# Optimization experiments

Hardware: AMD Instinct MI355X
Metric: run time of the kernel (lower is better)

Reference implementation:

```python
import jax, jax.numpy as jnp
import numpy as np
from jax import lax

C = 256
HEADS = 8
AREA = 4
MLP_DIM = int(1.2 * C)  # 307


def _conv1x1(x, w, s, b):
    # x: [B,C,H,W], w: [O,C], s,b: [O]  (Conv2d 1x1 bias=False + folded BN)
    y = jnp.einsum('bchw,oc->bohw', x, w)
    return y * s[None, :, None, None] + b[None, :, None, None]


def _dwconv3x3(x, w, s, b):
    # depthwise 3x3, groups=C; w: [C,1,3,3]
    y = lax.conv_general_dilated(x, w, (1, 1), ((1, 1), (1, 1)),
                                 feature_group_count=x.shape[1],
                                 dimension_numbers=('NCHW', 'OIHW', 'NCHW'))
    return y * s[None, :, None, None] + b[None, :, None, None]


def setup_inputs() -> dict:
    key = jax.random.key(0)
    ks = jax.random.split(key, 8)
    B, H, W = 2, 64, 64
    x = jax.random.normal(ks[0], (B, C, H, W), dtype=jnp.float32)
    std = 0.02
    w_qk = jax.random.normal(ks[1], (2 * C, C), dtype=jnp.float32) * std
    w_v = jax.random.normal(ks[2], (C, C), dtype=jnp.float32) * std
    w_pe = jax.random.normal(ks[3], (C, 1, 3, 3), dtype=jnp.float32) * std
    w_proj = jax.random.normal(ks[4], (C, C), dtype=jnp.float32) * std
    w_m1 = jax.random.normal(ks[5], (MLP_DIM, C), dtype=jnp.float32) * std
    w_m2 = jax.random.normal(ks[6], (C, MLP_DIM), dtype=jnp.float32) * std
    ones = lambda n: jnp.ones((n,), jnp.float32)
    zeros = lambda n: jnp.zeros((n,), jnp.float32)
    return {
        'x': x,
        'w_qk': w_qk, 's_qk': ones(2 * C), 'b_qk': zeros(2 * C),
        'w_v': w_v, 's_v': ones(C), 'b_v': zeros(C),
        'w_pe': w_pe, 's_pe': ones(C), 'b_pe': zeros(C),
        'w_proj': w_proj, 's_proj': ones(C), 'b_proj': zeros(C),
        'w_m1': w_m1, 's_m1': ones(MLP_DIM), 'b_m1': zeros(MLP_DIM),
        'w_m2': w_m2, 's_m2': ones(C), 'b_m2': zeros(C),
    }


def _block(x, w_qk, s_qk, b_qk, w_v, s_v, b_v, w_pe, s_pe, b_pe,
           w_proj, s_proj, b_proj, w_m1, s_m1, b_m1, w_m2, s_m2, b_m2):
    B, Cc, H, W = x.shape
    N = H * W
    hd = Cc // HEADS
    scale = hd ** -0.5

    # --- AreaAttention ---
    qk = _conv1x1(x, w_qk, s_qk, b_qk).reshape(B, 2 * Cc, N)
    v4 = _conv1x1(x, w_v, s_v, b_v)                 # [B,C,H,W]
    pe = _dwconv3x3(v4, w_pe, s_pe, b_pe)           # positional encoding
    v = v4.reshape(B, Cc, N)

    # area split (row-major reshape, identical to torch contiguous reshape)
    Ba, Na = B * AREA, N // AREA
    qk = qk.reshape(Ba, 2 * Cc, Na)
    v = v.reshape(Ba, Cc, Na)
    q, k = qk[:, :Cc], qk[:, Cc:]
    q = q.reshape(Ba, HEADS, hd, Na)
    k = k.reshape(Ba, HEADS, hd, Na)
    v = v.reshape(Ba, HEADS, hd, Na)

    attn = jnp.einsum('bhdn,bhdm->bhnm', q, k) * scale  # [Ba,H,Na,Na]
    attn = jax.nn.softmax(attn, axis=-1)
    out = jnp.einsum('bhdm,bhnm->bhdn', v, attn)         # [Ba,H,hd,Na]

    out = out.reshape(B, Cc, N).reshape(B, Cc, H, W)
    attn_out = _conv1x1(out + pe, w_proj, s_proj, b_proj)

    x1 = x + attn_out  # add=True (shortcut and in_c==out_c)

    # --- conv2 MLP: Conv(SiLU) -> Conv(act=False) ---
    m = jax.nn.silu(_conv1x1(x1, w_m1, s_m1, b_m1))
    m = _conv1x1(m, w_m2, s_m2, b_m2)
    return x1 + m


def reference(x, w_qk, s_qk, b_qk, w_v, s_v, b_v, w_pe, s_pe, b_pe,
              w_proj, s_proj, b_proj, w_m1, s_m1, b_m1, w_m2, s_m2, b_m2):
    return _block(x, w_qk, s_qk, b_qk, w_v, s_v, b_v, w_pe, s_pe, b_pe,
                  w_proj, s_proj, b_proj, w_m1, s_m1, b_m1, w_m2, s_m2, b_m2)
```

## Files before the change

### kernel.cpp

```cpp
#include <hip/hip_runtime.h>

typedef __attribute__((ext_vector_type(8))) short s8v;
typedef __attribute__((ext_vector_type(4))) float f4v;

#define QSC (0.17677669529663687f * 1.4426950408889634f)

__device__ __forceinline__ unsigned short f2bf(float x) {
    unsigned u = __float_as_uint(x);
    return (unsigned short)((u + 0x7fffu + ((u >> 16) & 1u)) >> 16);
}
__device__ __forceinline__ float bf2f(unsigned short h) {
    return __uint_as_float(((unsigned)h) << 16);
}
__device__ __forceinline__ unsigned trunc2(float a, float b) {
    return (__float_as_uint(b) & 0xffff0000u) | (__float_as_uint(a) >> 16);
}

__global__ __launch_bounds__(256) void wconv_kernel(
    const float* __restrict__ wqk, const float* __restrict__ sqk, const float* __restrict__ bqk,
    const float* __restrict__ wv,  const float* __restrict__ sv,  const float* __restrict__ bv,
    const float* __restrict__ wprj, const float* __restrict__ sprj,
    const float* __restrict__ wm1, const float* __restrict__ sm1, const float* __restrict__ bm1,
    const float* __restrict__ wm2, const float* __restrict__ sm2,
    const float* __restrict__ wpe9,
    unsigned short* __restrict__ Wqkv, unsigned short* __restrict__ Wp,
    unsigned short* __restrict__ Wm1,  unsigned short* __restrict__ Wm2,
    float* __restrict__ bpad, float* __restrict__ bqv, float* __restrict__ wpeT)
{
    int i = blockIdx.x * 256 + threadIdx.x;
    if (i < 196608) {
        int o = i >> 8, c = i & 255;
        float w;
        if (o < 512) { float f = ((o & 127) < 64) ? QSC : 1.f; w = wqk[i] * sqk[o] * f; }
        else          w = wv[(o - 512) * 256 + c] * sv[o - 512];
        Wqkv[i] = f2bf(w);
    } else if (i < 262144) {
        int j = i - 196608; int o = j >> 8; Wp[j] = f2bf(wprj[j] * sprj[o]);
    } else if (i < 360448) {
        int j = i - 262144; int o = j >> 8, c = j & 255;
        Wm1[j] = (o < 307) ? f2bf(wm1[o * 256 + c] * sm1[o]) : (unsigned short)0;
    } else if (i < 458752) {
        int j = i - 360448; int o = j / 384, c = j - o * 384;
        Wm2[j] = (c < 307) ? f2bf(wm2[o * 307 + c] * sm2[o]) : (unsigned short)0;
    } else if (i < 459136) {
        int j = i - 458752; bpad[j] = (j < 307) ? bm1[j] : 0.f;
    } else if (i < 459904) {
        int j = i - 459136;
        bqv[j] = (j < 512) ? (bqk[j] * (((j & 127) < 64) ? QSC : 1.f)) : bv[j - 512];
    } else if (i < 462208) {
        int j = i - 459904; int k = j >> 8, c = j & 255;
        wpeT[j] = wpe9[c * 9 + k];
    }
}

__global__ __launch_bounds__(256) void mmqkv_kernel(
    const float* __restrict__ X, const unsigned short* __restrict__ Wb,
    const float* __restrict__ bi,
    unsigned short* __restrict__ qP, unsigned short* __restrict__ kP,
    unsigned short* __restrict__ vC, unsigned short* __restrict__ vT)
{
    __shared__ unsigned short Ap[64][40];
    __shared__ unsigned short Wt[128][40];
    const int tid = threadIdx.x, lane = tid & 63, wv = tid >> 6;
    const int lo4 = lane & 15, quad = lane >> 4;
    const int p0 = blockIdx.x * 64, o0 = blockIdx.y * 128, bB = blockIdx.z;
    const int ph = (wv & 1) * 32, oh = (wv >> 1) * 64;
    const int c2 = tid & 15, pg = tid >> 4;
    const int oW0 = tid >> 2, oW1 = (tid + 256) >> 2;
    const int cW = (tid & 3) * 8;
    const float* xb = X + (size_t)bB * 256 * 4096;

    f4v acc[4][2];
    #pragma unroll
    for (int i = 0; i < 4; i++)
        #pragma unroll
        for (int j = 0; j < 2; j++)
            acc[i][j] = (f4v){0.f, 0.f, 0.f, 0.f};

    float4 fa = *(const float4*)&xb[(size_t)(2 * c2) * 4096 + p0 + pg * 4];
    float4 fb = *(const float4*)&xb[(size_t)(2 * c2 + 1) * 4096 + p0 + pg * 4];
    uint4 wReg0 = *(const uint4*)(Wb + (size_t)(o0 + oW0) * 256 + cW);
    uint4 wReg1 = *(const uint4*)(Wb + (size_t)(o0 + oW1) * 256 + cW);

    for (int kc = 0; kc < 8; kc++) {
        __syncthreads();
        {
            float av[4] = {fa.x, fa.y, fa.z, fa.w};
            float bv2[4] = {fb.x, fb.y, fb.z, fb.w};
            #pragma unroll
            for (int i = 0; i < 4; i++)
                *(unsigned*)&Ap[pg * 4 + i][2 * c2] =
                    (unsigned)f2bf(av[i]) | ((unsigned)f2bf(bv2[i]) << 16);
        }
        *(uint4*)&Wt[oW0][cW] = wReg0;
        *(uint4*)&Wt[oW1][cW] = wReg1;
        __syncthreads();
        if (kc < 7) {
            int k1 = (kc + 1) * 32;
            fa = *(const float4*)&xb[(size_t)(k1 + 2 * c2) * 4096 + p0 + pg * 4];
            fb = *(const float4*)&xb[(size_t)(k1 + 2 * c2 + 1) * 4096 + p0 + pg * 4];
            wReg0 = *(const uint4*)(Wb + (size_t)(o0 + oW0) * 256 + k1 + cW);
            wReg1 = *(const uint4*)(Wb + (size_t)(o0 + oW1) * 256 + k1 + cW);
        }
        s8v af[4], bx[2];
        #pragma unroll
        for (int of = 0; of < 4; of++)
            af[of] = *(const s8v*)&Wt[oh + of * 16 + lo4][quad * 8];
        #pragma unroll
        for (int pf = 0; pf < 2; pf++)
            bx[pf] = *(const s8v*)&Ap[ph + pf * 16 + lo4][quad * 8];
        #pragma unroll
        for (int of = 0; of < 4; of++)
            #pragma unroll
            for (int pf = 0; pf < 2; pf++)
                acc[of][pf] = __builtin_amdgcn_mfma_f32_16x16x32_bf16(af[of], bx[pf], acc[of][pf], 0, 0, 0);
    }
    #pragma unroll
    for (int of = 0; of < 4; of++) {
        int ob = o0 + oh + of * 16 + quad * 4;
        float4 bb = *(const float4*)&bi[ob];
        float bbv[4] = {bb.x, bb.y, bb.z, bb.w};
        #pragma unroll
        for (int pf = 0; pf < 2; pf++) {
            int p = p0 + ph + pf * 16 + lo4;
            unsigned short b4[4];
            #pragma unroll
            for (int r = 0; r < 4; r++) b4[r] = f2bf(acc[of][pf][r] + bbv[r]);
            if (ob < 512) {
                int gg = ob >> 7, rr = ob & 127;
                int hh = (rr & 63) >> 3, j0 = rr & 7;
                unsigned short* dst = (rr >= 64) ? kP : qP;
                *(ushort4*)&dst[((((size_t)(bB * 4 + gg)) * 8 + hh) * 1024 + (p & 1023)) * 32
                                + (p >> 10) * 8 + j0] = *(ushort4*)b4;
            } else {
                *(ushort4*)&vC[((size_t)(bB * 4096 + p)) * 256 + (ob - 512)] = *(ushort4*)b4;
                #pragma unroll
                for (int r = 0; r < 4; r++)
                    vT[((size_t)(bB * 256 + ob - 512 + r)) * 4096 + p] = b4[r];
            }
        }
    }
}

__global__ __launch_bounds__(256) void attn_kernel(
    const unsigned short* __restrict__ qP, const unsigned short* __restrict__ kP,
    const unsigned short* __restrict__ vT,
    unsigned short* __restrict__ Opart, float* __restrict__ Lpart)
{
    __shared__ unsigned short Pq[4][2][32][64];
    const int tid = threadIdx.x;
    const int w = tid >> 6, lane = tid & 63;
    const int lo4 = lane & 15, quad = lane >> 4;
    const int swz = (lo4 & 7) << 4;
    const int n0 = blockIdx.z * 128;
    const int h = blockIdx.y;
    const int z = blockIdx.x;
    const int ba = z >> 1, spl = z & 1;
    const int bB = ba >> 2, g = ba & 3;
    const int mbase = spl * 512;

    const unsigned short* qb = qP + (((size_t)(bB * 4) + g) * 8 + h) * 32768;
    const unsigned short* kb = kP + (((size_t)(bB * 4) + g) * 8 + h) * 32768;

    s8v qf[2];
    #pragma unroll
    for (int qc = 0; qc < 2; qc++)
        qf[qc] = *(const s8v*)(qb + (size_t)(n0 + w * 32 + qc * 16 + lo4) * 32 + quad * 8);
    const int dd0 = lo4, dd1 = 16 + lo4;
    const unsigned short* vb0 = vT + ((size_t)(bB * 256 + g * 64 + h * 8 + (dd0 & 7))) * 4096 + (dd0 >> 3) * 1024 + mbase + quad * 8;
    const unsigned short* vb1 = vT + ((size_t)(bB * 256 + g * 64 + h * 8 + (dd1 & 7))) * 4096 + (dd1 >> 3) * 1024 + mbase + quad * 8;

    f4v oacc[2][2], Lacc[2];
    #pragma unroll
    for (int i = 0; i < 2; i++) {
        Lacc[i] = (f4v){0.f, 0.f, 0.f, 0.f};
        #pragma unroll
        for (int j = 0; j < 2; j++)
            oacc[i][j] = (f4v){0.f, 0.f, 0.f, 0.f};
    }
    s8v ones;
    #pragma unroll
    for (int j = 0; j < 8; j++) ones[j] = (short)0x3F80;

    s8v kf[4], vCur[2][2];
    #pragma unroll
    for (int mf = 0; mf < 4; mf++)
        kf[mf] = *(const s8v*)(kb + (size_t)(mbase + mf * 16 + lo4) * 32 + quad * 8);

    #pragma unroll
    for (int sc = 0; sc < 8; sc++) {
        s8v vNew[2][2];
        #pragma unroll
        for (int mc = 0; mc < 2; mc++) {
            vNew[mc][0] = *(const s8v*)(vb0 + sc * 64 + mc * 32);
            vNew[mc][1] = *(const s8v*)(vb1 + sc * 64 + mc * 32);
        }
        s8v kfn[4];
        if (sc < 7) {
            #pragma unroll
            for (int mf = 0; mf < 4; mf++)
                kfn[mf] = *(const s8v*)(kb + (size_t)(mbase + (sc + 1) * 64 + mf * 16 + lo4) * 32 + quad * 8);
        }
        f4v sT[4][2];
        __builtin_amdgcn_s_setprio(1);
        #pragma unroll
        for (int mf = 0; mf < 4; mf++)
            #pragma unroll
            for (int qc = 0; qc < 2; qc++)
                sT[mf][qc] = __builtin_amdgcn_mfma_f32_16x16x32_bf16(kf[mf], qf[qc], (f4v){0.f, 0.f, 0.f, 0.f}, 0, 0, 0);
        __builtin_amdgcn_s_setprio(0);
        #pragma unroll
        for (int qc = 0; qc < 2; qc++) {
            char* prow = (char*)&Pq[w][sc & 1][qc * 16 + lo4][0];
            #pragma unroll
            for (int mf = 0; mf < 4; mf++) {
                float p0v = exp2f(sT[mf][qc][0]);
                float p1v = exp2f(sT[mf][qc][1]);
                float p2v = exp2f(sT[mf][qc][2]);
                float p3v = exp2f(sT[mf][qc][3]);
                uint2 pk;
                pk.x = trunc2(p0v, p1v);
                pk.y = trunc2(p2v, p3v);
                *(uint2*)(prow + ((mf * 32 + quad * 8) ^ swz)) = pk;
            }
        }
        if (sc > 0) {
            #pragma unroll
            for (int mc = 0; mc < 2; mc++) {
                s8v pfr[2];
                #pragma unroll
                for (int qc = 0; qc < 2; qc++)
                    pfr[qc] = *(const s8v*)((const char*)&Pq[w][(sc - 1) & 1][qc * 16 + lo4][0] + ((mc * 64 + quad * 16) ^ swz));
                __builtin_amdgcn_s_setprio(1);
                #pragma unroll
                for (int df = 0; df < 2; df++)
                    #pragma unroll
                    for (int qc = 0; qc < 2; qc++)
                        oacc[df][qc] = __builtin_amdgcn_mfma_f32_16x16x32_bf16(vCur[mc][df], pfr[qc], oacc[df][qc], 0, 0, 0);
                #pragma unroll
                for (int qc = 0; qc < 2; qc++)
                    Lacc[qc] = __builtin_amdgcn_mfma_f32_16x16x32_bf16(ones, pfr[qc], Lacc[qc], 0, 0, 0);
                __builtin_amdgcn_s_setprio(0);
            }
        }
        if (sc < 7) {
            #pragma unroll
            for (int mf = 0; mf < 4; mf++) kf[mf] = kfn[mf];
        }
        #pragma unroll
        for (int mc = 0; mc < 2; mc++) {
            vCur[mc][0] = vNew[mc][0];
            vCur[mc][1] = vNew[mc][1];
        }
    }
    #pragma unroll
    for (int mc = 0; mc < 2; mc++) {
        s8v pfr[2];
        #pragma unroll
        for (int qc = 0; qc < 2; qc++)
            pfr[qc] = *(const s8v*)((const char*)&Pq[w][1][qc * 16 + lo4][0] + ((mc * 64 + quad * 16) ^ swz));
        __builtin_amdgcn_s_setprio(1);
        #pragma unroll
        for (int df = 0; df < 2; df++)
            #pragma unroll
            for (int qc = 0; qc < 2; qc++)
                oacc[df][qc] = __builtin_amdgcn_mfma_f32_16x16x32_bf16(vCur[mc][df], pfr[qc], oacc[df][qc], 0, 0, 0);
        #pragma unroll
        for (int qc = 0; qc < 2; qc++)
            Lacc[qc] = __builtin_amdgcn_mfma_f32_16x16x32_bf16(ones, pfr[qc], Lacc[qc], 0, 0, 0);
        __builtin_amdgcn_s_setprio(0);
    }
    if (quad == 0) {
        size_t lb = (((size_t)(spl * 2 + bB) * 4 + g) * 8 + h) * 1024 + n0 + w * 32;
        Lpart[lb + lo4] = Lacc[0][0];
        Lpart[lb + 16 + lo4] = Lacc[1][0];
    }
    #pragma unroll
    for (int qc = 0; qc < 2; qc++)
        #pragma unroll
        for (int df = 0; df < 2; df++) {
            int pb = df * 2 + (quad >> 1);
            uint2 ov;
            ov.x = trunc2(oacc[df][qc][0], oacc[df][qc][1]);
            ov.y = trunc2(oacc[df][qc][2], oacc[df][qc][3]);
            *(uint2*)(Opart + ((size_t)(spl * 2 + bB) * 4096 + pb * 1024 + n0 + w * 32 + qc * 16 + lo4) * 256
                      + g * 64 + h * 8 + (quad & 1) * 4) = ov;
        }
}

__global__ __launch_bounds__(256) void attpe_kernel(
    const unsigned short* __restrict__ Opart, const float* __restrict__ Lpart,
    const unsigned short* __restrict__ vC, const float* __restrict__ wpeT,
    const float* __restrict__ spe, const float* __restrict__ bpe,
    unsigned short* __restrict__ attpe)
{
    int idx = blockIdx.x * 256 + threadIdx.x;
    int cg = (idx & 31) * 8;
    int p = (idx >> 5) & 4095;
    int bB = idx >> 17;
    int g = cg >> 6, h = (cg >> 3) & 7;
    int na = p & 1023;
    float L = 0.f;
    float o[8] = {};
    #pragma unroll
    for (int spl = 0; spl < 2; spl++) {
        L += Lpart[(((size_t)(spl * 2 + bB) * 4 + g) * 8 + h) * 1024 + na];
        uint4 v = *(const uint4*)(Opart + ((size_t)(spl * 2 + bB) * 4096 + p) * 256 + cg);
        unsigned short tmp[8]; *(uint4*)tmp = v;
        #pragma unroll
        for (int j = 0; j < 8; j++) o[j] += bf2f(tmp[j]);
    }
    float inv = 1.f / L;
    int hh = p >> 6, ww = p & 63;
    float pe[8] = {};
    for (int di = -1; di <= 1; di++) {
        int h2 = hh + di;
        if (h2 < 0 || h2 > 63) continue;
        for (int dj = -1; dj <= 1; dj++) {
            int w2 = ww + dj;
            if (w2 < 0 || w2 > 63) continue;
            uint4 vv = *(const uint4*)(vC + ((size_t)(bB * 4096 + h2 * 64 + w2)) * 256 + cg);
            unsigned short tmp[8]; *(uint4*)tmp = vv;
            int k = (di + 1) * 3 + (dj + 1);
            float4 wa = *(const float4*)&wpeT[k * 256 + cg];
            float4 wb = *(const float4*)&wpeT[k * 256 + cg + 4];
            float ww8[8] = {wa.x, wa.y, wa.z, wa.w, wb.x, wb.y, wb.z, wb.w};
            #pragma unroll
            for (int j = 0; j < 8; j++)
                pe[j] = fmaf(bf2f(tmp[j]), ww8[j], pe[j]);
        }
    }
    float4 sa = *(const float4*)&spe[cg];
    float4 sb = *(const float4*)&spe[cg + 4];
    float4 b0 = *(const float4*)&bpe[cg];
    float4 b1 = *(const float4*)&bpe[cg + 4];
    float sv8[8] = {sa.x, sa.y, sa.z, sa.w, sb.x, sb.y, sb.z, sb.w};
    float bv8[8] = {b0.x, b0.y, b0.z, b0.w, b1.x, b1.y, b1.z, b1.w};
    unsigned short ob[8];
    #pragma unroll
    for (int j = 0; j < 8; j++)
        ob[j] = f2bf(o[j] * inv + pe[j] * sv8[j] + bv8[j]);
    *(uint4*)(attpe + ((size_t)(bB * 4096 + p)) * 256 + cg) = *(uint4*)ob;
}

__global__ __launch_bounds__(512) void mlp3_kernel(
    const unsigned short* __restrict__ attpe, const float* __restrict__ x,
    const unsigned short* __restrict__ Wp, const float* __restrict__ bp,
    const unsigned short* __restrict__ Wm1, const float* __restrict__ bm1p,
    const unsigned short* __restrict__ Wm2, const float* __restrict__ bm2,
    float* __restrict__ out)
{
    __shared__ unsigned short bufA[16][392];
    __shared__ unsigned short bufX[16][264];
    const int tid = threadIdx.x, lane = tid & 63, wv = tid >> 6;
    const int lo4 = lane & 15, quad = lane >> 4;
    const int p0 = blockIdx.x * 16, bB = blockIdx.y;

    {
        int row = tid >> 5, cb = (tid & 31) * 8;
        *(uint4*)&bufA[row][cb] =
            *(const uint4*)(attpe + ((size_t)(bB * 4096 + p0 + row)) * 256 + cb);
    }
    __syncthreads();

    {
        f4v acc[2] = {(f4v){0.f, 0.f, 0.f, 0.f}, (f4v){0.f, 0.f, 0.f, 0.f}};
        for (int kk = 0; kk < 8; kk++) {
            s8v bx = *(const s8v*)&bufA[lo4][kk * 32 + quad * 8];
            #pragma unroll
            for (int of = 0; of < 2; of++) {
                s8v af = *(const s8v*)(Wp + (size_t)(wv * 32 + of * 16 + lo4) * 256 + kk * 32 + quad * 8);
                acc[of] = __builtin_amdgcn_mfma_f32_16x16x32_bf16(af, bx, acc[of], 0, 0, 0);
            }
        }
        #pragma unroll
        for (int of = 0; of < 2; of++) {
            int ob = wv * 32 + of * 16 + quad * 4;
            float4 bb = *(const float4*)&bp[ob];
            float bbv[4] = {bb.x, bb.y, bb.z, bb.w};
            int p = p0 + lo4;
            unsigned short b4[4];
            #pragma unroll
            for (int r = 0; r < 4; r++) {
                float y = acc[of][r] + bbv[r] + x[((size_t)(bB * 256 + ob + r)) * 4096 + p];
                b4[r] = f2bf(y);
            }
            *(ushort4*)&bufX[lo4][ob] = *(ushort4*)b4;
        }
    }
    __syncthreads();

    {
        f4v acc[3] = {(f4v){0.f, 0.f, 0.f, 0.f}, (f4v){0.f, 0.f, 0.f, 0.f}, (f4v){0.f, 0.f, 0.f, 0.f}};
        for (int kk = 0; kk < 8; kk++) {
            s8v bx = *(const s8v*)&bufX[lo4][kk * 32 + quad * 8];
            #pragma unroll
            for (int of = 0; of < 3; of++) {
                s8v af = *(const s8v*)(Wm1 + (size_t)(wv * 48 + of * 16 + lo4) * 256 + kk * 32 + quad * 8);
                acc[of] = __builtin_amdgcn_mfma_f32_16x16x32_bf16(af, bx, acc[of], 0, 0, 0);
            }
        }
        #pragma unroll
        for (int of = 0; of < 3; of++) {
            int ob = wv * 48 + of * 16 + quad * 4;
            float4 bb = *(const float4*)&bm1p[ob];
            float bbv[4] = {bb.x, bb.y, bb.z, bb.w};
            unsigned short b4[4];
            #pragma unroll
            for (int r = 0; r < 4; r++) {
                float y = acc[of][r] + bbv[r];
                y = y / (1.f + __expf(-y));
                b4[r] = f2bf(y);
            }
            *(ushort4*)&bufA[lo4][ob] = *(ushort4*)b4;
        }
    }
    __syncthreads();

    {
        f4v acc[2] = {(f4v){0.f, 0.f, 0.f, 0.f}, (f4v){0.f, 0.f, 0.f, 0.f}};
        for (int kk = 0; kk < 12; kk++) {
            s8v bx = *(const s8v*)&bufA[lo4][kk * 32 + quad * 8];
            #pragma unroll
            for (int of = 0; of < 2; of++) {
                s8v af = *(const s8v*)(Wm2 + (size_t)(wv * 32 + of * 16 + lo4) * 384 + kk * 32 + quad * 8);
                acc[of] = __builtin_amdgcn_mfma_f32_16x16x32_bf16(af, bx, acc[of], 0, 0, 0);
            }
        }
        #pragma unroll
        for (int of = 0; of < 2; of++) {
            int ob = wv * 32 + of * 16 + quad * 4;
            float4 bb = *(const float4*)&bm2[ob];
            float bbv[4] = {bb.x, bb.y, bb.z, bb.w};
            ushort4 x1v = *(const ushort4*)&bufX[lo4][ob];
            unsigned short x1a[4]; *(ushort4*)x1a = x1v;
            #pragma unroll
            for (int r = 0; r < 4; r++) {
                float y = acc[of][r] + bbv[r] + bf2f(x1a[r]);
                out[((size_t)(bB * 256 + ob + r)) * 4096 + p0 + lo4] = y;
            }
        }
    }
}

extern "C" void kernel_launch(void* const* d_in, const int* in_sizes, int n_in,
                              void* d_out, int out_size, void* d_ws, size_t ws_size,
                              hipStream_t stream)
{
    const float* x      = (const float*)d_in[0];
    const float* w_qk   = (const float*)d_in[1];
    const float* s_qk   = (const float*)d_in[2];
    const float* b_qk   = (const float*)d_in[3];
    const float* w_v    = (const float*)d_in[4];
    const float* s_v    = (const float*)d_in[5];
    const float* b_v    = (const float*)d_in[6];
    const float* w_pe   = (const float*)d_in[7];
    const float* s_pe   = (const float*)d_in[8];
    const float* b_pe   = (const float*)d_in[9];
    const float* w_proj = (const float*)d_in[10];
    const float* s_proj = (const float*)d_in[11];
    const float* b_proj = (const float*)d_in[12];
    const float* w_m1   = (const float*)d_in[13];
    const float* s_m1   = (const float*)d_in[14];
    const float* b_m1   = (const float*)d_in[15];
    const float* w_m2   = (const float*)d_in[16];
    const float* s_m2   = (const float*)d_in[17];
    const float* b_m2   = (const float*)d_in[18];
    float* out = (float*)d_out;

    const size_t NA = (size_t)2 * 4096 * 256;
    unsigned short* attpe = (unsigned short*)d_ws;
    unsigned short* vC   = attpe + NA;
    unsigned short* qP   = vC + NA;
    unsigned short* kP   = qP + NA;
    unsigned short* Opart = kP + NA;
    float* Lpart = (float*)(Opart + 2 * NA);
    unsigned short* Wqkv = (unsigned short*)(Lpart + 131072);
    unsigned short* Wp   = Wqkv + 196608;
    unsigned short* Wm1  = Wp + 65536;
    unsigned short* Wm2  = Wm1 + 98304;
    float* bpad = (float*)(Wm2 + 98304);
    float* bqv  = bpad + 384;
    float* wpeT = bqv + 768;
    unsigned short* vT = (unsigned short*)(wpeT + 2304);

    dim3 blk(256);
    wconv_kernel<<<dim3(1806), blk, 0, stream>>>(
        w_qk, s_qk, b_qk, w_v, s_v, b_v, w_proj, s_proj,
        w_m1, s_m1, b_m1, w_m2, s_m2, w_pe,
        Wqkv, Wp, Wm1, Wm2, bpad, bqv, wpeT);

    mmqkv_kernel<<<dim3(64, 6, 2), blk, 0, stream>>>(x, Wqkv, bqv, qP, kP, vC, vT);

    attn_kernel<<<dim3(16, 8, 8), blk, 0, stream>>>(qP, kP, vT, Opart, Lpart);
    attpe_kernel<<<dim3(1024), blk, 0, stream>>>(Opart, Lpart, vC, wpeT, s_pe, b_pe, attpe);

    mlp3_kernel<<<dim3(256, 2), dim3(512), 0, stream>>>(
        attpe, x, Wp, b_proj, Wm1, bpad, Wm2, b_m2, out);
}
```

Baseline: 177.2 us.

## Drop split-K attention partials and pre-convert X to bf16 in prep kernel

The attention kernel no longer splits the key dimension into two halves. Each block now handles 64 queries over all 1024 keys, normalises by the row sum in-kernel, and writes a single bf16 output. This removes the Opart/Lpart partial buffers and the reduction step in attpe. Separately, the weight-prep kernel now converts X to bf16 so the QKV GEMM loads half the bytes; the price is an extra full pass over X in a larger prep launch. Per-block work in attention changes from 128 queries over 512 keys to 64 queries over 1024 keys, which gives longer serial loops per wave but the same block count.

```diff
diff --git a/kernel.cpp b/kernel.cpp
--- a/kernel.cpp
+++ b/kernel.cpp
@@ -22,10 +22,11 @@
     const float* __restrict__ wprj, const float* __restrict__ sprj,
     const float* __restrict__ wm1, const float* __restrict__ sm1, const float* __restrict__ bm1,
     const float* __restrict__ wm2, const float* __restrict__ sm2,
-    const float* __restrict__ wpe9,
+    const float* __restrict__ wpe9, const float* __restrict__ X,
     unsigned short* __restrict__ Wqkv, unsigned short* __restrict__ Wp,
     unsigned short* __restrict__ Wm1,  unsigned short* __restrict__ Wm2,
-    float* __restrict__ bpad, float* __restrict__ bqv, float* __restrict__ wpeT)
+    float* __restrict__ bpad, float* __restrict__ bqv, float* __restrict__ wpeT,
+    unsigned short* __restrict__ xbf)
 {
     int i = blockIdx.x * 256 + threadIdx.x;
     if (i < 196608) {
@@ -50,11 +51,14 @@
     } else if (i < 462208) {
         int j = i - 459904; int k = j >> 8, c = j & 255;
         wpeT[j] = wpe9[c * 9 + k];
+    } else if (i < 2559360) {
+        int j = i - 462208;
+        xbf[j] = f2bf(X[j]);
     }
 }
 
 __global__ __launch_bounds__(256) void mmqkv_kernel(
-    const float* __restrict__ X, const unsigned short* __restrict__ Wb,
+    const unsigned short* __restrict__ Xbf, const unsigned short* __restrict__ Wb,
     const float* __restrict__ bi,
     unsigned short* __restrict__ qP, unsigned short* __restrict__ kP,
     unsigned short* __restrict__ vC, unsigned short* __restrict__ vT)
@@ -68,7 +72,7 @@
     const int c2 = tid & 15, pg = tid >> 4;
     const int oW0 = tid >> 2, oW1 = (tid + 256) >> 2;
     const int cW = (tid & 3) * 8;
-    const float* xb = X + (size_t)bB * 256 * 4096;
+    const unsigned short* xb = Xbf + (size_t)bB * 256 * 4096;
 
     f4v acc[4][2];
     #pragma unroll
@@ -77,28 +81,28 @@
         for (int j = 0; j < 2; j++)
             acc[i][j] = (f4v){0.f, 0.f, 0.f, 0.f};
 
-    float4 fa = *(const float4*)&xb[(size_t)(2 * c2) * 4096 + p0 + pg * 4];
-    float4 fb = *(const float4*)&xb[(size_t)(2 * c2 + 1) * 4096 + p0 + pg * 4];
+    ushort4 fa = *(const ushort4*)&xb[(size_t)(2 * c2) * 4096 + p0 + pg * 4];
+    ushort4 fb = *(const ushort4*)&xb[(size_t)(2 * c2 + 1) * 4096 + p0 + pg * 4];
     uint4 wReg0 = *(const uint4*)(Wb + (size_t)(o0 + oW0) * 256 + cW);
     uint4 wReg1 = *(const uint4*)(Wb + (size_t)(o0 + oW1) * 256 + cW);
 
     for (int kc = 0; kc < 8; kc++) {
         __syncthreads();
         {
-            float av[4] = {fa.x, fa.y, fa.z, fa.w};
-            float bv2[4] = {fb.x, fb.y, fb.z, fb.w};
+            unsigned short av[4] = {fa.x, fa.y, fa.z, fa.w};
+            unsigned short bv2[4] = {fb.x, fb.y, fb.z, fb.w};
             #pragma unroll
             for (int i = 0; i < 4; i++)
                 *(unsigned*)&Ap[pg * 4 + i][2 * c2] =
-                    (unsigned)f2bf(av[i]) | ((unsigned)f2bf(bv2[i]) << 16);
+                    (unsigned)av[i] | ((unsigned)bv2[i] << 16);
         }
         *(uint4*)&Wt[oW0][cW] = wReg0;
         *(uint4*)&Wt[oW1][cW] = wReg1;
         __syncthreads();
         if (kc < 7) {
             int k1 = (kc + 1) * 32;
-            fa = *(const float4*)&xb[(size_t)(k1 + 2 * c2) * 4096 + p0 + pg * 4];
-            fb = *(const float4*)&xb[(size_t)(k1 + 2 * c2 + 1) * 4096 + p0 + pg * 4];
+            fa = *(const ushort4*)&xb[(size_t)(k1 + 2 * c2) * 4096 + p0 + pg * 4];
+            fb = *(const ushort4*)&xb[(size_t)(k1 + 2 * c2 + 1) * 4096 + p0 + pg * 4];
             wReg0 = *(const uint4*)(Wb + (size_t)(o0 + oW0) * 256 + k1 + cW);
             wReg1 = *(const uint4*)(Wb + (size_t)(o0 + oW1) * 256 + k1 + cW);
         }
@@ -145,39 +149,29 @@
 __global__ __launch_bounds__(256) void attn_kernel(
     const unsigned short* __restrict__ qP, const unsigned short* __restrict__ kP,
     const unsigned short* __restrict__ vT,
-    unsigned short* __restrict__ Opart, float* __restrict__ Lpart)
-{
-    __shared__ unsigned short Pq[4][2][32][64];
+    unsigned short* __restrict__ attO)
+{
+    __shared__ unsigned short Pq[4][2][16][64];
     const int tid = threadIdx.x;
     const int w = tid >> 6, lane = tid & 63;
     const int lo4 = lane & 15, quad = lane >> 4;
     const int swz = (lo4 & 7) << 4;
-    const int n0 = blockIdx.z * 128;
-    const int h = blockIdx.y;
-    const int z = blockIdx.x;
-    const int ba = z >> 1, spl = z & 1;
+    const int ba = blockIdx.x >> 3, h = blockIdx.x & 7;
+    const int n0 = blockIdx.y * 64;
     const int bB = ba >> 2, g = ba & 3;
-    const int mbase = spl * 512;
 
     const unsigned short* qb = qP + (((size_t)(bB * 4) + g) * 8 + h) * 32768;
     const unsigned short* kb = kP + (((size_t)(bB * 4) + g) * 8 + h) * 32768;
 
-    s8v qf[2];
-    #pragma unroll
-    for (int qc = 0; qc < 2; qc++)
-        qf[qc] = *(const s8v*)(qb + (size_t)(n0 + w * 32 + qc * 16 + lo4) * 32 + quad * 8);
+    s8v qf = *(const s8v*)(qb + (size_t)(n0 + w * 16 + lo4) * 32 + quad * 8);
     const int dd0 = lo4, dd1 = 16 + lo4;
-    const unsigned short* vb0 = vT + ((size_t)(bB * 256 + g * 64 + h * 8 + (dd0 & 7))) * 4096 + (dd0 >> 3) * 1024 + mbase + quad * 8;
-    const unsigned short* vb1 = vT + ((size_t)(bB * 256 + g * 64 + h * 8 + (dd1 & 7))) * 4096 + (dd1 >> 3) * 1024 + mbase + quad * 8;
-
-    f4v oacc[2][2], Lacc[2];
-    #pragma unroll
-    for (int i = 0; i < 2; i++) {
-        Lacc[i] = (f4v){0.f, 0.f, 0.f, 0.f};
-        #pragma unroll
-        for (int j = 0; j < 2; j++)
-            oacc[i][j] = (f4v){0.f, 0.f, 0.f, 0.f};
-    }
+    const unsigned short* vb0 = vT + ((size_t)(bB * 256 + g * 64 + h * 8 + (dd0 & 7))) * 4096 + (dd0 >> 3) * 1024 + quad * 8;
+    const unsigned short* vb1 = vT + ((size_t)(bB * 256 + g * 64 + h * 8 + (dd1 & 7))) * 4096 + (dd1 >> 3) * 1024 + quad * 8;
+
+    f4v oacc[2], Lacc;
+    oacc[0] = (f4v){0.f, 0.f, 0.f, 0.f};
+    oacc[1] = (f4v){0.f, 0.f, 0.f, 0.f};
+    Lacc    = (f4v){0.f, 0.f, 0.f, 0.f};
     s8v ones;
     #pragma unroll
     for (int j = 0; j < 8; j++) ones[j] = (short)0x3F80;
@@ -185,10 +179,10 @@
     s8v kf[4], vCur[2][2];
     #pragma unroll
     for (int mf = 0; mf < 4; mf++)
-        kf[mf] = *(const s8v*)(kb + (size_t)(mbase + mf * 16 + lo4) * 32 + quad * 8);
-
-    #pragma unroll
-    for (int sc = 0; sc < 8; sc++) {
+        kf[mf] = *(const s8v*)(kb + (size_t)(mf * 16 + lo4) * 32 + quad * 8);
+
+    #pragma unroll
+    for (int sc = 0; sc < 16; sc++) {
         s8v vNew[2][2];
         #pragma unroll
         for (int mc = 0; mc < 2; mc++) {
@@ -196,28 +190,25 @@
             vNew[mc][1] = *(const s8v*)(vb1 + sc * 64 + mc * 32);
         }
         s8v kfn[4];
-        if (sc < 7) {
+        if (sc < 15) {
             #pragma unroll
             for (int mf = 0; mf < 4; mf++)
-                kfn[mf] = *(const s8v*)(kb + (size_t)(mbase + (sc + 1) * 64 + mf * 16 + lo4) * 32 + quad * 8);
-        }
-        f4v sT[4][2];
+                kfn[mf] = *(const s8v*)(kb + (size_t)((sc + 1) * 64 + mf * 16 + lo4) * 32 + quad * 8);
+        }
+        f4v sT[4];
         __builtin_amdgcn_s_setprio(1);
         #pragma unroll
         for (int mf = 0; mf < 4; mf++)
-            #pragma unroll
-            for (int qc = 0; qc < 2; qc++)
-                sT[mf][qc] = __builtin_amdgcn_mfma_f32_16x16x32_bf16(kf[mf], qf[qc], (f4v){0.f, 0.f, 0.f, 0.f}, 0, 0, 0);
+            sT[mf] = __builtin_amdgcn_mfma_f32_16x16x32_bf16(kf[mf], qf, (f4v){0.f, 0.f, 0.f, 0.f}, 0, 0, 0);
         __builtin_amdgcn_s_setprio(0);
-        #pragma unroll
-        for (int qc = 0; qc < 2; qc++) {
-            char* prow = (char*)&Pq[w][sc & 1][qc * 16 + lo4][0];
+        {
+            char* prow = (char*)&Pq[w][sc & 1][lo4][0];
             #pragma unroll
             for (int mf = 0; mf < 4; mf++) {
-                float p0v = exp2f(sT[mf][qc][0]);
-                float p1v = exp2f(sT[mf][qc][1]);
-                float p2v = exp2f(sT[mf][qc][2]);
-                float p3v = exp2f(sT[mf][qc][3]);
+                float p0v = exp2f(sT[mf][0]);
+                float p1v = exp2f(sT[mf][1]);
+                float p2v = exp2f(sT[mf][2]);
+                float p3v = exp2f(sT[mf][3]);
                 uint2 pk;
                 pk.x = trunc2(p0v, p1v);
                 pk.y = trunc2(p2v, p3v);
@@ -227,23 +218,15 @@
         if (sc > 0) {
             #pragma unroll
             for (int mc = 0; mc < 2; mc++) {
-                s8v pfr[2];
-                #pragma unroll
-                for (int qc = 0; qc < 2; qc++)
-                    pfr[qc] = *(const s8v*)((const char*)&Pq[w][(sc - 1) & 1][qc * 16 + lo4][0] + ((mc * 64 + quad * 16) ^ swz));
+                s8v pfr = *(const s8v*)((const char*)&Pq[w][(sc - 1) & 1][lo4][0] + ((mc * 64 + quad * 16) ^ swz));
                 __builtin_amdgcn_s_setprio(1);
-                #pragma unroll
-                for (int df = 0; df < 2; df++)
-                    #pragma unroll
-                    for (int qc = 0; qc < 2; qc++)
-                        oacc[df][qc] = __builtin_amdgcn_mfma_f32_16x16x32_bf16(vCur[mc][df], pfr[qc], oacc[df][qc], 0, 0, 0);
-                #pragma unroll
-                for (int qc = 0; qc < 2; qc++)
-                    Lacc[qc] = __builtin_amdgcn_mfma_f32_16x16x32_bf16(ones, pfr[qc], Lacc[qc], 0, 0, 0);
+                oacc[0] = __builtin_amdgcn_mfma_f32_16x16x32_bf16(vCur[mc][0], pfr, oacc[0], 0, 0, 0);
+                oacc[1] = __builtin_amdgcn_mfma_f32_16x16x32_bf16(vCur[mc][1], pfr, oacc[1], 0, 0, 0);
+                Lacc    = __builtin_amdgcn_mfma_f32_16x16x32_bf16(ones, pfr, Lacc, 0, 0, 0);
                 __builtin_amdgcn_s_setprio(0);
             }
         }
-        if (sc < 7) {
+        if (sc < 15) {
             #pragma unroll
             for (int mf = 0; mf < 4; mf++) kf[mf] = kfn[mf];
         }
@@ -255,41 +238,27 @@
     }
     #pragma unroll
     for (int mc = 0; mc < 2; mc++) {
-        s8v pfr[2];
-        #pragma unroll
-        for (int qc = 0; qc < 2; qc++)
-            pfr[qc] = *(const s8v*)((const char*)&Pq[w][1][qc * 16 + lo4][0] + ((mc * 64 + quad * 16) ^ swz));
+        s8v pfr = *(const s8v*)((const char*)&Pq[w][1][lo4][0] + ((mc * 64 + quad * 16) ^ swz));
         __builtin_amdgcn_s_setprio(1);
-        #pragma unroll
-        for (int df = 0; df < 2; df++)
-            #pragma unroll
-            for (int qc = 0; qc < 2; qc++)
-                oacc[df][qc] = __builtin_amdgcn_mfma_f32_16x16x32_bf16(vCur[mc][df], pfr[qc], oacc[df][qc], 0, 0, 0);
-        #pragma unroll
-        for (int qc = 0; qc < 2; qc++)
-            Lacc[qc] = __builtin_amdgcn_mfma_f32_16x16x32_bf16(ones, pfr[qc], Lacc[qc], 0, 0, 0);
+        oacc[0] = __builtin_amdgcn_mfma_f32_16x16x32_bf16(vCur[mc][0], pfr, oacc[0], 0, 0, 0);
+        oacc[1] = __builtin_amdgcn_mfma_f32_16x16x32_bf16(vCur[mc][1], pfr, oacc[1], 0, 0, 0);
+        Lacc    = __builtin_amdgcn_mfma_f32_16x16x32_bf16(ones, pfr, Lacc, 0, 0, 0);
         __builtin_amdgcn_s_setprio(0);
     }
-    if (quad == 0) {
-        size_t lb = (((size_t)(spl * 2 + bB) * 4 + g) * 8 + h) * 1024 + n0 + w * 32;
-        Lpart[lb + lo4] = Lacc[0][0];
-        Lpart[lb + 16 + lo4] = Lacc[1][0];
-    }
-    #pragma unroll
-    for (int qc = 0; qc < 2; qc++)
-        #pragma unroll
-        for (int df = 0; df < 2; df++) {
-            int pb = df * 2 + (quad >> 1);
-            uint2 ov;
-            ov.x = trunc2(oacc[df][qc][0], oacc[df][qc][1]);
-            ov.y = trunc2(oacc[df][qc][2], oacc[df][qc][3]);
-            *(uint2*)(Opart + ((size_t)(spl * 2 + bB) * 4096 + pb * 1024 + n0 + w * 32 + qc * 16 + lo4) * 256
-                      + g * 64 + h * 8 + (quad & 1) * 4) = ov;
-        }
+    float inv = 1.f / Lacc[0];
+    #pragma unroll
+    for (int df = 0; df < 2; df++) {
+        int pb = df * 2 + (quad >> 1);
+        uint2 ov;
+        ov.x = trunc2(oacc[df][0] * inv, oacc[df][1] * inv);
+        ov.y = trunc2(oacc[df][2] * inv, oacc[df][3] * inv);
+        *(uint2*)(attO + ((size_t)(bB * 4096) + pb * 1024 + n0 + w * 16 + lo4) * 256
+                  + g * 64 + h * 8 + (quad & 1) * 4) = ov;
+    }
 }
 
 __global__ __launch_bounds__(256) void attpe_kernel(
-    const unsigned short* __restrict__ Opart, const float* __restrict__ Lpart,
+    const unsigned short* __restrict__ attO,
     const unsigned short* __restrict__ vC, const float* __restrict__ wpeT,
     const float* __restrict__ spe, const float* __restrict__ bpe,
     unsigned short* __restrict__ attpe)
@@ -298,19 +267,13 @@
     int cg = (idx & 31) * 8;
     int p = (idx >> 5) & 4095;
     int bB = idx >> 17;
-    int g = cg >> 6, h = (cg >> 3) & 7;
-    int na = p & 1023;
-    float L = 0.f;
-    float o[8] = {};
-    #pragma unroll
-    for (int spl = 0; spl < 2; spl++) {
-        L += Lpart[(((size_t)(spl * 2 + bB) * 4 + g) * 8 + h) * 1024 + na];
-        uint4 v = *(const uint4*)(Opart + ((size_t)(spl * 2 + bB) * 4096 + p) * 256 + cg);
+    float o[8];
+    {
+        uint4 v = *(const uint4*)(attO + ((size_t)(bB * 4096 + p)) * 256 + cg);
         unsigned short tmp[8]; *(uint4*)tmp = v;
         #pragma unroll
-        for (int j = 0; j < 8; j++) o[j] += bf2f(tmp[j]);
-    }
-    float inv = 1.f / L;
+        for (int j = 0; j < 8; j++) o[j] = bf2f(tmp[j]);
+    }
     int hh = p >> 6, ww = p & 63;
     float pe[8] = {};
     for (int di = -1; di <= 1; di++) {
@@ -339,7 +302,7 @@
     unsigned short ob[8];
     #pragma unroll
     for (int j = 0; j < 8; j++)
-        ob[j] = f2bf(o[j] * inv + pe[j] * sv8[j] + bv8[j]);
+        ob[j] = f2bf(o[j] + pe[j] * sv8[j] + bv8[j]);
     *(uint4*)(attpe + ((size_t)(bB * 4096 + p)) * 256 + cg) = *(uint4*)ob;
 }
 
@@ -473,27 +436,27 @@
     unsigned short* vC   = attpe + NA;
     unsigned short* qP   = vC + NA;
     unsigned short* kP   = qP + NA;
-    unsigned short* Opart = kP + NA;
-    float* Lpart = (float*)(Opart + 2 * NA);
-    unsigned short* Wqkv = (unsigned short*)(Lpart + 131072);
+    unsigned short* attO = kP + NA;
+    unsigned short* xbf  = attO + NA;
+    unsigned short* vT   = xbf + NA;
+    unsigned short* Wqkv = vT + NA;
     unsigned short* Wp   = Wqkv + 196608;
     unsigned short* Wm1  = Wp + 65536;
     unsigned short* Wm2  = Wm1 + 98304;
     float* bpad = (float*)(Wm2 + 98304);
     float* bqv  = bpad + 384;
     float* wpeT = bqv + 768;
-    unsigned short* vT = (unsigned short*)(wpeT + 2304);
 
     dim3 blk(256);
-    wconv_kernel<<<dim3(1806), blk, 0, stream>>>(
+    wconv_kernel<<<dim3(9998), blk, 0, stream>>>(
         w_qk, s_qk, b_qk, w_v, s_v, b_v, w_proj, s_proj,
-        w_m1, s_m1, b_m1, w_m2, s_m2, w_pe,
-        Wqkv, Wp, Wm1, Wm2, bpad, bqv, wpeT);
-
-    mmqkv_kernel<<<dim3(64, 6, 2), blk, 0, stream>>>(x, Wqkv, bqv, qP, kP, vC, vT);
-
-    attn_kernel<<<dim3(16, 8, 8), blk, 0, stream>>>(qP, kP, vT, Opart, Lpart);
-    attpe_kernel<<<dim3(1024), blk, 0, stream>>>(Opart, Lpart, vC, wpeT, s_pe, b_pe, attpe);
+        w_m1, s_m1, b_m1, w_m2, s_m2, w_pe, x,
+        Wqkv, Wp, Wm1, Wm2, bpad, bqv, wpeT, xbf);
+
+    mmqkv_kernel<<<dim3(64, 6, 2), blk, 0, stream>>>(xbf, Wqkv, bqv, qP, kP, vC, vT);
+
+    attn_kernel<<<dim3(64, 16), blk, 0, stream>>>(qP, kP, vT, attO);
+    attpe_kernel<<<dim3(1024), blk, 0, stream>>>(attO, vC, wpeT, s_pe, b_pe, attpe);
 
     mlp3_kernel<<<dim3(256, 2), dim3(512), 0, stream>>>(
         attpe, x, Wp, b_proj, Wm1, bpad, Wm2, b_m2, out);
```

Measured after the change: 198.7 us. 1.12x slower.

## Fuse attention merge and PE into MLP kernel; pre-convert x to bf16

Applied to the files above, without the earlier changes.

The separate attpe kernel, which merged the two split-softmax partials, normalized them and added the depthwise 3x3 positional encoding, is folded into the prologue of mlp3_kernel. This removes one launch and the round trip of the attpe intermediate through global memory. Separately, x is converted to bf16 once in the weight-prep kernel, so the QKV GEMM loads half the bytes and skips per-tile conversion. The cost is an extra full pass over x in the prep kernel, and the fused MLP prologue now does the 9-tap gather per block.

```diff
diff --git a/kernel.cpp b/kernel.cpp
--- a/kernel.cpp
+++ b/kernel.cpp
@@ -22,10 +22,11 @@
     const float* __restrict__ wprj, const float* __restrict__ sprj,
     const float* __restrict__ wm1, const float* __restrict__ sm1, const float* __restrict__ bm1,
     const float* __restrict__ wm2, const float* __restrict__ sm2,
-    const float* __restrict__ wpe9,
+    const float* __restrict__ wpe9, const float* __restrict__ X,
     unsigned short* __restrict__ Wqkv, unsigned short* __restrict__ Wp,
     unsigned short* __restrict__ Wm1,  unsigned short* __restrict__ Wm2,
-    float* __restrict__ bpad, float* __restrict__ bqv, float* __restrict__ wpeT)
+    float* __restrict__ bpad, float* __restrict__ bqv, float* __restrict__ wpeT,
+    unsigned short* __restrict__ xbf)
 {
     int i = blockIdx.x * 256 + threadIdx.x;
     if (i < 196608) {
@@ -50,11 +51,14 @@
     } else if (i < 462208) {
         int j = i - 459904; int k = j >> 8, c = j & 255;
         wpeT[j] = wpe9[c * 9 + k];
+    } else if (i < 2559360) {
+        int j = i - 462208;
+        xbf[j] = f2bf(X[j]);
     }
 }
 
 __global__ __launch_bounds__(256) void mmqkv_kernel(
-    const float* __restrict__ X, const unsigned short* __restrict__ Wb,
+    const unsigned short* __restrict__ Xbf, const unsigned short* __restrict__ Wb,
     const float* __restrict__ bi,
     unsigned short* __restrict__ qP, unsigned short* __restrict__ kP,
     unsigned short* __restrict__ vC, unsigned short* __restrict__ vT)
@@ -68,7 +72,7 @@
     const int c2 = tid & 15, pg = tid >> 4;
     const int oW0 = tid >> 2, oW1 = (tid + 256) >> 2;
     const int cW = (tid & 3) * 8;
-    const float* xb = X + (size_t)bB * 256 * 4096;
+    const unsigned short* xb = Xbf + (size_t)bB * 256 * 4096;
 
     f4v acc[4][2];
     #pragma unroll
@@ -77,28 +81,28 @@
         for (int j = 0; j < 2; j++)
             acc[i][j] = (f4v){0.f, 0.f, 0.f, 0.f};
 
-    float4 fa = *(const float4*)&xb[(size_t)(2 * c2) * 4096 + p0 + pg * 4];
-    float4 fb = *(const float4*)&xb[(size_t)(2 * c2 + 1) * 4096 + p0 + pg * 4];
+    ushort4 fa = *(const ushort4*)&xb[(size_t)(2 * c2) * 4096 + p0 + pg * 4];
+    ushort4 fb = *(const ushort4*)&xb[(size_t)(2 * c2 + 1) * 4096 + p0 + pg * 4];
     uint4 wReg0 = *(const uint4*)(Wb + (size_t)(o0 + oW0) * 256 + cW);
     uint4 wReg1 = *(const uint4*)(Wb + (size_t)(o0 + oW1) * 256 + cW);
 
     for (int kc = 0; kc < 8; kc++) {
         __syncthreads();
         {
-            float av[4] = {fa.x, fa.y, fa.z, fa.w};
-            float bv2[4] = {fb.x, fb.y, fb.z, fb.w};
+            unsigned short av[4] = {fa.x, fa.y, fa.z, fa.w};
+            unsigned short bv2[4] = {fb.x, fb.y, fb.z, fb.w};
             #pragma unroll
             for (int i = 0; i < 4; i++)
                 *(unsigned*)&Ap[pg * 4 + i][2 * c2] =
-                    (unsigned)f2bf(av[i]) | ((unsigned)f2bf(bv2[i]) << 16);
+                    (unsigned)av[i] | ((unsigned)bv2[i] << 16);
         }
         *(uint4*)&Wt[oW0][cW] = wReg0;
         *(uint4*)&Wt[oW1][cW] = wReg1;
         __syncthreads();
         if (kc < 7) {
             int k1 = (kc + 1) * 32;
-            fa = *(const float4*)&xb[(size_t)(k1 + 2 * c2) * 4096 + p0 + pg * 4];
-            fb = *(const float4*)&xb[(size_t)(k1 + 2 * c2 + 1) * 4096 + p0 + pg * 4];
+            fa = *(const ushort4*)&xb[(size_t)(k1 + 2 * c2) * 4096 + p0 + pg * 4];
+            fb = *(const ushort4*)&xb[(size_t)(k1 + 2 * c2 + 1) * 4096 + p0 + pg * 4];
             wReg0 = *(const uint4*)(Wb + (size_t)(o0 + oW0) * 256 + k1 + cW);
             wReg1 = *(const uint4*)(Wb + (size_t)(o0 + oW1) * 256 + k1 + cW);
         }
@@ -288,63 +292,11 @@
         }
 }
 
-__global__ __launch_bounds__(256) void attpe_kernel(
+__global__ __launch_bounds__(512) void mlp3_kernel(
     const unsigned short* __restrict__ Opart, const float* __restrict__ Lpart,
     const unsigned short* __restrict__ vC, const float* __restrict__ wpeT,
     const float* __restrict__ spe, const float* __restrict__ bpe,
-    unsigned short* __restrict__ attpe)
-{
-    int idx = blockIdx.x * 256 + threadIdx.x;
-    int cg = (idx & 31) * 8;
-    int p = (idx >> 5) & 4095;
-    int bB = idx >> 17;
-    int g = cg >> 6, h = (cg >> 3) & 7;
-    int na = p & 1023;
-    float L = 0.f;
-    float o[8] = {};
-    #pragma unroll
-    for (int spl = 0; spl < 2; spl++) {
-        L += Lpart[(((size_t)(spl * 2 + bB) * 4 + g) * 8 + h) * 1024 + na];
-        uint4 v = *(const uint4*)(Opart + ((size_t)(spl * 2 + bB) * 4096 + p) * 256 + cg);
-        unsigned short tmp[8]; *(uint4*)tmp = v;
-        #pragma unroll
-        for (int j = 0; j < 8; j++) o[j] += bf2f(tmp[j]);
-    }
-    float inv = 1.f / L;
-    int hh = p >> 6, ww = p & 63;
-    float pe[8] = {};
-    for (int di = -1; di <= 1; di++) {
-        int h2 = hh + di;
-        if (h2 < 0 || h2 > 63) continue;
-        for (int dj = -1; dj <= 1; dj++) {
-            int w2 = ww + dj;
-            if (w2 < 0 || w2 > 63) continue;
-            uint4 vv = *(const uint4*)(vC + ((size_t)(bB * 4096 + h2 * 64 + w2)) * 256 + cg);
-            unsigned short tmp[8]; *(uint4*)tmp = vv;
-            int k = (di + 1) * 3 + (dj + 1);
-            float4 wa = *(const float4*)&wpeT[k * 256 + cg];
-            float4 wb = *(const float4*)&wpeT[k * 256 + cg + 4];
-            float ww8[8] = {wa.x, wa.y, wa.z, wa.w, wb.x, wb.y, wb.z, wb.w};
-            #pragma unroll
-            for (int j = 0; j < 8; j++)
-                pe[j] = fmaf(bf2f(tmp[j]), ww8[j], pe[j]);
-        }
-    }
-    float4 sa = *(const float4*)&spe[cg];
-    float4 sb = *(const float4*)&spe[cg + 4];
-    float4 b0 = *(const float4*)&bpe[cg];
-    float4 b1 = *(const float4*)&bpe[cg + 4];
-    float sv8[8] = {sa.x, sa.y, sa.z, sa.w, sb.x, sb.y, sb.z, sb.w};
-    float bv8[8] = {b0.x, b0.y, b0.z, b0.w, b1.x, b1.y, b1.z, b1.w};
-    unsigned short ob[8];
-    #pragma unroll
-    for (int j = 0; j < 8; j++)
-        ob[j] = f2bf(o[j] * inv + pe[j] * sv8[j] + bv8[j]);
-    *(uint4*)(attpe + ((size_t)(bB * 4096 + p)) * 256 + cg) = *(uint4*)ob;
-}
-
-__global__ __launch_bounds__(512) void mlp3_kernel(
-    const unsigned short* __restrict__ attpe, const float* __restrict__ x,
+    const float* __restrict__ x,
     const unsigned short* __restrict__ Wp, const float* __restrict__ bp,
     const unsigned short* __restrict__ Wm1, const float* __restrict__ bm1p,
     const unsigned short* __restrict__ Wm2, const float* __restrict__ bm2,
@@ -357,9 +309,51 @@
     const int p0 = blockIdx.x * 16, bB = blockIdx.y;
 
     {
-        int row = tid >> 5, cb = (tid & 31) * 8;
-        *(uint4*)&bufA[row][cb] =
-            *(const uint4*)(attpe + ((size_t)(bB * 4096 + p0 + row)) * 256 + cb);
+        int row = tid >> 5, cg = (tid & 31) * 8;
+        int p = p0 + row;
+        int g = cg >> 6, h = (cg >> 3) & 7;
+        int na = p & 1023;
+        float L = 0.f;
+        float o[8] = {};
+        #pragma unroll
+        for (int spl = 0; spl < 2; spl++) {
+            L += Lpart[(((size_t)(spl * 2 + bB) * 4 + g) * 8 + h) * 1024 + na];
+            uint4 v = *(const uint4*)(Opart + ((size_t)(spl * 2 + bB) * 4096 + p) * 256 + cg);
+            unsigned short tmp[8]; *(uint4*)tmp = v;
+            #pragma unroll
+            for (int j = 0; j < 8; j++) o[j] += bf2f(tmp[j]);
+        }
+        float inv = 1.f / L;
+        int hh = p >> 6, ww = p & 63;
+        float pe[8] = {};
+        for (int di = -1; di <= 1; di++) {
+            int h2 = hh + di;
+            if (h2 < 0 || h2 > 63) continue;
+            for (int dj = -1; dj <= 1; dj++) {
+                int w2 = ww + dj;
+                if (w2 < 0 || w2 > 63) continue;
+                uint4 vv = *(const uint4*)(vC + ((size_t)(bB * 4096 + h2 * 64 + w2)) * 256 + cg);
+                unsigned short tmp[8]; *(uint4*)tmp = vv;
+                int k = (di + 1) * 3 + (dj + 1);
+                float4 wa = *(const float4*)&wpeT[k * 256 + cg];
+                float4 wb = *(const float4*)&wpeT[k * 256 + cg + 4];
+                float ww8[8] = {wa.x, wa.y, wa.z, wa.w, wb.x, wb.y, wb.z, wb.w};
+                #pragma unroll
+                for (int j = 0; j < 8; j++)
+                    pe[j] = fmaf(bf2f(tmp[j]), ww8[j], pe[j]);
+            }
+        }
+        float4 sa = *(const float4*)&spe[cg];
+        float4 sb = *(const float4*)&spe[cg + 4];
+        float4 b0 = *(const float4*)&bpe[cg];
+        float4 b1 = *(const float4*)&bpe[cg + 4];
+        float sv8[8] = {sa.x, sa.y, sa.z, sa.w, sb.x, sb.y, sb.z, sb.w};
+        float bv8[8] = {b0.x, b0.y, b0.z, b0.w, b1.x, b1.y, b1.z, b1.w};
+        unsigned short ob8[8];
+        #pragma unroll
+        for (int j = 0; j < 8; j++)
+            ob8[j] = f2bf(o[j] * inv + pe[j] * sv8[j] + bv8[j]);
+        *(uint4*)&bufA[row][cg] = *(uint4*)ob8;
     }
     __syncthreads();
 
@@ -469,32 +463,32 @@
     float* out = (float*)d_out;
 
     const size_t NA = (size_t)2 * 4096 * 256;
-    unsigned short* attpe = (unsigned short*)d_ws;
-    unsigned short* vC   = attpe + NA;
+    unsigned short* vC   = (unsigned short*)d_ws;
     unsigned short* qP   = vC + NA;
     unsigned short* kP   = qP + NA;
     unsigned short* Opart = kP + NA;
     float* Lpart = (float*)(Opart + 2 * NA);
-    unsigned short* Wqkv = (unsigned short*)(Lpart + 131072);
+    unsigned short* xbf  = (unsigned short*)(Lpart + 131072);
+    unsigned short* vT   = xbf + NA;
+    unsigned short* Wqkv = vT + NA;
     unsigned short* Wp   = Wqkv + 196608;
     unsigned short* Wm1  = Wp + 65536;
     unsigned short* Wm2  = Wm1 + 98304;
     float* bpad = (float*)(Wm2 + 98304);
     float* bqv  = bpad + 384;
     float* wpeT = bqv + 768;
-    unsigned short* vT = (unsigned short*)(wpeT + 2304);
 
     dim3 blk(256);
-    wconv_kernel<<<dim3(1806), blk, 0, stream>>>(
+    wconv_kernel<<<dim3(9998), blk, 0, stream>>>(
         w_qk, s_qk, b_qk, w_v, s_v, b_v, w_proj, s_proj,
-        w_m1, s_m1, b_m1, w_m2, s_m2, w_pe,
-        Wqkv, Wp, Wm1, Wm2, bpad, bqv, wpeT);
-
-    mmqkv_kernel<<<dim3(64, 6, 2), blk, 0, stream>>>(x, Wqkv, bqv, qP, kP, vC, vT);
+        w_m1, s_m1, b_m1, w_m2, s_m2, w_pe, x,
+        Wqkv, Wp, Wm1, Wm2, bpad, bqv, wpeT, xbf);
+
+    mmqkv_kernel<<<dim3(64, 6, 2), blk, 0, stream>>>(xbf, Wqkv, bqv, qP, kP, vC, vT);
 
     attn_kernel<<<dim3(16, 8, 8), blk, 0, stream>>>(qP, kP, vT, Opart, Lpart);
-    attpe_kernel<<<dim3(1024), blk, 0, stream>>>(Opart, Lpart, vC, wpeT, s_pe, b_pe, attpe);
 
     mlp3_kernel<<<dim3(256, 2), dim3(512), 0, stream>>>(
-        attpe, x, Wp, b_proj, Wm1, bpad, Wm2, b_m2, out);
-}
+        Opart, Lpart, vC, wpeT, s_pe, b_pe,
+        x, Wp, b_proj, Wm1, bpad, Wm2, b_m2, out);
+}
```

New measurement: 179.5 us. About the same (+1.3%).
